# Optimization experiments

Measured on AMD Instinct MI355X. Metric: run time of the kernel, lower is better.

## Reference

```python
import jax, jax.numpy as jnp
import numpy as np

# ---- shape constants (d_data=1, expand_factor=1) ----
B, L, DD = 32, 8192, 1
M, NL = 3, 2                      # 3 Mamba control nets, n_layers=2 each
DM = 4 * DD                       # mamba d_model = 4*d_data
DI = DM                           # d_inner = expand_factor * d_model
NS = 16                           # d_state
KC = 4                            # d_conv
DR = max(1, -(-DM // 16))         # dt_rank = ceil(d_model/16)
DT = 1e-4                         # forward scalar arg dt (fixed python float)
TAU = 1000.0
SMOOTH = int(round(0.001 / DT))   # smooth_len/dt = 10

# 9-point (8th order) central finite-difference coefficients for f' (no 1/dt)
_C1 = [1/280, -4/105, 1/5, -4/5, 0.0, 4/5, -1/5, 4/105, -1/280]

def deriv_approx_dy(x):
    Lp = x.shape[1] - 8
    return sum(c * x[:, k:k + Lp, :] for k, c in enumerate(_C1) if c != 0.0)

def smooth(x, k):
    # centered box filter, same output length (via cumsum sliding window)
    if k <= 1:
        return x
    xp = jnp.pad(x, ((0, 0), ((k - 1) // 2 + 1, k // 2), (0, 0)))
    c = jnp.cumsum(xp, axis=1)
    return (c[:, k:, :] - c[:, :-k, :]) / k

def rmsnorm(x, w):
    return x * jax.lax.rsqrt(jnp.mean(x * x, -1, keepdims=True) + 1e-5) * w

def causal_conv(u, w, b):
    # depthwise causal conv == torch Conv1d(groups=DI, padding=KC-1)[..., :L]
    Lc = u.shape[1]
    up = jnp.pad(u, ((0, 0), (KC - 1, 0), (0, 0)))
    y = sum(up[:, j:j + Lc, :] * w[:, j] for j in range(KC))
    return y + b

def selective_scan(u, delta, A, Bm, Cm, Dp):
    # u, delta: [b,l,di]; A: [di,ns]; Bm, Cm: [b,l,ns]; Dp: [di]
    dA = jnp.exp(delta[..., None] * A)                         # [b,l,di,ns]
    dBu = delta[..., None] * Bm[:, :, None, :] * u[..., None]  # [b,l,di,ns]
    def step(h, xs):
        a, bu = xs
        h = a * h + bu
        return h, h
    h0 = jnp.zeros((u.shape[0], DI, NS), u.dtype)
    _, hs = jax.lax.scan(step, h0, (jnp.moveaxis(dA, 1, 0), jnp.moveaxis(dBu, 1, 0)))
    hs = jnp.moveaxis(hs, 0, 1)                                # [b,l,di,ns]
    return jnp.einsum('bldn,bln->bld', hs, Cm) + u * Dp

def _run_mamba(x_in, m, in_proj_w, conv_w, conv_b, x_proj_w,
               dt_proj_w, dt_proj_b, A_log, D_param, norm_w, out_proj_w):
    h = x_in
    for l in range(NL):
        hn = rmsnorm(h, norm_w[m, l])
        xz = hn @ in_proj_w[m, l].T                            # [b,l,2*di]
        xc, res = jnp.split(xz, 2, axis=-1)
        xc = jax.nn.silu(causal_conv(xc, conv_w[m, l], conv_b[m, l]))
        dbc = xc @ x_proj_w[m, l].T
        dtr, Bm, Cm = dbc[..., :DR], dbc[..., DR:DR + NS], dbc[..., DR + NS:]
        delta = jax.nn.softplus(dtr @ dt_proj_w[m, l].T + dt_proj_b[m, l])
        A = -jnp.exp(A_log[m, l])
        y = selective_scan(xc, delta, A, Bm, Cm, D_param[m, l])
        y = y * jax.nn.silu(res)
        h = y @ out_proj_w[m, l].T + h                         # residual block
    return h

def _forward(x, in_proj_w, conv_w, conv_b, x_proj_w, dt_proj_w, dt_proj_b,
             A_log, D_param, norm_w, out_proj_w, omega_w, omega_b,
             gamma_w, gamma_b, d_w, d_b, b_param):
    xdot = deriv_approx_dy(x)                                  # [B, L-8, DD]
    z = jnp.concatenate([x[:, 4:-4, :], xdot], axis=-1)        # [B, L', 2]
    x_in = jnp.concatenate([z, jnp.flip(z, axis=1)], axis=-1)  # [B, L', 4]
    args = (in_proj_w, conv_w, conv_b, x_proj_w, dt_proj_w, dt_proj_b,
            A_log, D_param, norm_w, out_proj_w)
    omegaC = _run_mamba(x_in, 0, *args)
    gammaC = _run_mamba(x_in, 1, *args)
    dC = _run_mamba(x_in, 2, *args)
    b = jax.nn.relu(b_param) / TAU
    d = jax.nn.relu(dC @ d_w.T + d_b)
    omega = omegaC @ omega_w.T + omega_b
    gamma = (gammaC @ gamma_w.T + gamma_b) / TAU
    d = smooth(jnp.abs(d), SMOOTH)
    omega = smooth(jnp.abs(omega), SMOOTH)
    gamma = smooth(gamma, SMOOTH)
    z = jnp.concatenate([z[:, :, :-1], z[:, :, -1:] / DT], axis=-1)
    z1, z2 = z[:, :, :1], z[:, :, 1:]
    yhat = -omega ** 2 * z1 + gamma * z2 - b * (z1 ** 2) * z2 - d
    def pen(t):
        # torch.var(dim=1) is unbiased -> ddof=1
        return jnp.mean(jnp.var(jnp.diff(t, axis=1)[:, 1:, :], axis=1, ddof=1))
    penalty = (pen(omega) + pen(gamma) + pen(d)) / 3.0
    controls = jnp.concatenate([omegaC, gammaC, dC], axis=-1)
    return yhat, controls, penalty

def setup_inputs():
    key = jax.random.key(0)
    ks = jax.random.split(key, 16)
    f32 = jnp.float32
    def nrm(k, shape, s=0.1):
        return s * jax.random.normal(k, shape, f32)
    x = jax.random.normal(ks[0], (B, L, DD), f32)
    A_log = jnp.log(jnp.broadcast_to(jnp.arange(1, NS + 1, dtype=f32), (M, NL, DI, NS)))
    return {
        "x": x,
        "in_proj_w": nrm(ks[1], (M, NL, 2 * DI, DM)),
        "conv_w": nrm(ks[2], (M, NL, DI, KC)),
        "conv_b": nrm(ks[3], (M, NL, DI)),
        "x_proj_w": nrm(ks[4], (M, NL, DR + 2 * NS, DI)),
        "dt_proj_w": nrm(ks[5], (M, NL, DI, DR)),
        "dt_proj_b": nrm(ks[6], (M, NL, DI)),
        "A_log": A_log,
        "D_param": jnp.ones((M, NL, DI), f32),
        "norm_w": jnp.ones((M, NL, DM), f32),
        "out_proj_w": nrm(ks[7], (M, NL, DM, DI)),
        "omega_w": nrm(ks[8], (DD, DM)),
        "omega_b": nrm(ks[9], (DD,)),
        "gamma_w": nrm(ks[10], (DD, DM)),
        "gamma_b": nrm(ks[11], (DD,)),
        "d_w": nrm(ks[12], (DD, DM)),
        "d_b": nrm(ks[13], (DD,)),
        "b_param": jax.random.uniform(ks[14], (1,), f32),
    }

def reference(x, in_proj_w, conv_w, conv_b, x_proj_w, dt_proj_w, dt_proj_b,
              A_log, D_param, norm_w, out_proj_w, omega_w, omega_b,
              gamma_w, gamma_b, d_w, d_b, b_param):
    return _forward(x, in_proj_w, conv_w, conv_b, x_proj_w, dt_proj_w, dt_proj_b,
                    A_log, D_param, norm_w, out_proj_w, omega_w, omega_b,
                    gamma_w, gamma_b, d_w, d_b, b_param)
```

## Files before the change

### kernel.cpp

```cpp
#include <hip/hip_runtime.h>
#include <math.h>

#define Bn_   32
#define Ln_   8192
#define LCn   8184
#define NLn   2
#define NCHn  341
#define CHn   24
#define NGn   24

static constexpr long N_BL = (long)Bn_ * LCn;

static constexpr long OFF_H    = 0;
static constexpr long OFF_REC  = 12*N_BL;
static constexpr long OFF_YB   = 36*N_BL;
static constexpr long OFF_RAW  = OFF_REC;
static constexpr long OFF_PART = OFF_REC + 3*N_BL;

#define L2E_  1.4426950408889634f
#define LN2_  0.6931471805599453f
#define EXP2_(x) __builtin_amdgcn_exp2f(x)
#define LOG2_(x) __builtin_amdgcn_logf(x)

__device__ __forceinline__ float si_(float v) {
    float e = EXP2_(-v * L2E_);
    return v * __builtin_amdgcn_rcpf(1.f + e);
}

__device__ __forceinline__ float sel4(float4 v, int d) {
    return (d & 2) ? ((d & 1) ? v.w : v.z) : ((d & 1) ? v.y : v.x);
}

__device__ __forceinline__ float rowsum16(float p) {
    p += __int_as_float(__builtin_amdgcn_update_dpp(0, __float_as_int(p), 0x128, 0xF, 0xF, true));
    p += __int_as_float(__builtin_amdgcn_update_dpp(0, __float_as_int(p), 0x124, 0xF, 0xF, true));
    p += __int_as_float(__builtin_amdgcn_update_dpp(0, __float_as_int(p), 0x122, 0xF, 0xF, true));
    p += __int_as_float(__builtin_amdgcn_update_dpp(0, __float_as_int(p), 0x121, 0xF, 0xF, true));
    return p;
}

__global__ void k_prep(const float* __restrict__ x, float* __restrict__ xin) {
    long idx = (long)blockIdx.x * 256 + threadIdx.x;
    if (idx >= N_BL) return;
    int b = (int)(idx / LCn);
    int t = (int)(idx - (long)b * LCn);
    const float* xb = x + (long)b * Ln_;
    const float c0 = 1.f/280.f, c1 = -4.f/105.f, c2 = 0.2f, c3 = -0.8f,
                c5 = 0.8f, c6 = -0.2f, c7 = 4.f/105.f, c8 = -1.f/280.f;
    float xd  = c0*xb[t]   + c1*xb[t+1] + c2*xb[t+2] + c3*xb[t+3]
              + c5*xb[t+5] + c6*xb[t+6] + c7*xb[t+7] + c8*xb[t+8];
    float z0  = xb[t+4];
    int tf = LCn - 1 - t;
    float xdf = c0*xb[tf]   + c1*xb[tf+1] + c2*xb[tf+2] + c3*xb[tf+3]
              + c5*xb[tf+5] + c6*xb[tf+6] + c7*xb[tf+7] + c8*xb[tf+8];
    float zf0 = xb[tf+4];
    float4 v; v.x = z0; v.y = xd; v.z = zf0; v.w = xdf;
    *(float4*)(xin + idx*4) = v;
}

__global__ void k_preconv(const float* __restrict__ hin, long mstride, int l,
                          const float* __restrict__ ipw, const float* __restrict__ cw,
                          const float* __restrict__ cbv, const float* __restrict__ nw,
                          const float* __restrict__ xpw, const float* __restrict__ dtw,
                          const float* __restrict__ dtb, float* __restrict__ rec) {
    long idx = (long)blockIdx.x * 256 + threadIdx.x;
    if (idx >= 3*N_BL) return;
    int m = (int)(idx / N_BL);
    long r = idx - (long)m * N_BL;
    int bb = (int)(r / LCn);
    int t  = (int)(r - (long)bb * LCn);
    int ml = m*NLn + l;
    const float* hb = hin + (long)m*mstride + (long)bb*LCn*4;
    const float* W  = ipw + (long)ml*32;
    const float* wn = nw  + ml*4;
    const float* wc = cw  + ml*16;
    const float* bc = cbv + ml*4;
    float acc0=0.f, acc1=0.f, acc2=0.f, acc3=0.f;
#pragma unroll
    for (int j = 0; j < 4; j++) {
        int tt = t - 3 + j;
        if (tt < 0) continue;
        float4 hv = *(const float4*)(hb + (long)tt*4);
        float ms = (hv.x*hv.x + hv.y*hv.y + hv.z*hv.z + hv.w*hv.w)*0.25f + 1e-5f;
        float rs = __builtin_amdgcn_rsqf(ms);
        float hn0 = hv.x*rs*wn[0], hn1 = hv.y*rs*wn[1];
        float hn2 = hv.z*rs*wn[2], hn3 = hv.w*rs*wn[3];
        float x0 = W[0]*hn0 + W[1]*hn1 + W[2]*hn2 + W[3]*hn3;
        float x1 = W[4]*hn0 + W[5]*hn1 + W[6]*hn2 + W[7]*hn3;
        float x2 = W[8]*hn0 + W[9]*hn1 + W[10]*hn2 + W[11]*hn3;
        float x3 = W[12]*hn0 + W[13]*hn1 + W[14]*hn2 + W[15]*hn3;
        acc0 = fmaf(x0, wc[0*4+j], acc0);
        acc1 = fmaf(x1, wc[1*4+j], acc1);
        acc2 = fmaf(x2, wc[2*4+j], acc2);
        acc3 = fmaf(x3, wc[3*4+j], acc3);
    }
    float4 o;
    o.x = si_(acc0 + bc[0]); o.y = si_(acc1 + bc[1]);
    o.z = si_(acc2 + bc[2]); o.w = si_(acc3 + bc[3]);
    const float* P = xpw + (long)ml*33*4;
    float dtr = o.x*P[0] + o.y*P[1] + o.z*P[2] + o.w*P[3];
    const float* dwv = dtw + ml*4;
    const float* dbv = dtb + ml*4;
    float4 lg;
    lg.x = LOG2_(1.f + EXP2_(fmaf(dtr, dwv[0], dbv[0]) * L2E_));
    lg.y = LOG2_(1.f + EXP2_(fmaf(dtr, dwv[1], dbv[1]) * L2E_));
    lg.z = LOG2_(1.f + EXP2_(fmaf(dtr, dwv[2], dbv[2]) * L2E_));
    lg.w = LOG2_(1.f + EXP2_(fmaf(dtr, dwv[3], dbv[3]) * L2E_));
    float* rp = rec + ((long)m*N_BL + r)*8;
    *(float4*)rp       = o;
    *(float4*)(rp + 4) = lg;
}

__global__ __launch_bounds__(256, 8)
void k_scanB(const float* __restrict__ rec, int l,
             const float* __restrict__ xpw, const float* __restrict__ Alog,
             float* __restrict__ Ap, float* __restrict__ Sv) {
    int wid  = blockIdx.x*4 + (threadIdx.x >> 6);
    int lane = threadIdx.x & 63;
    int chunk = wid % NCHn;
    int g     = wid / NCHn;
    int m = g >> 3;
    int s = lane >> 4, n = lane & 15;
    int bb = (g & 7)*4 + s;
    int ml = m*NLn + l;
    const float* P  = xpw + (long)ml*33*4;
    const float* PB = P + (1+n)*4;
    float pb0 = PB[0]*LN2_, pb1 = PB[1]*LN2_, pb2 = PB[2]*LN2_, pb3 = PB[3]*LN2_;
    const float* AL = Alog + (long)ml*64 + n;
    float4 Av;
    Av.x = -EXP2_(AL[0]  * L2E_);
    Av.y = -EXP2_(AL[16] * L2E_);
    Av.z = -EXP2_(AL[32] * L2E_);
    Av.w = -EXP2_(AL[48] * L2E_);
    const float* rb = rec + ((long)m*N_BL + (long)bb*LCn)*8;
    int t0 = chunk*CHn;
    float4 ap; ap.x = ap.y = ap.z = ap.w = 1.f;
    float4 sv; sv.x = sv.y = sv.z = sv.w = 0.f;
#pragma unroll 4
    for (int t = t0; t < t0 + CHn; t++) {
        float4 u  = *(const float4*)(rb + (long)t*8);
        float4 lg = *(const float4*)(rb + (long)t*8 + 4);
        float Bv = u.x*pb0 + u.y*pb1 + u.z*pb2 + u.w*pb3;
        float4 a;
        a.x = EXP2_(lg.x * Av.x); a.y = EXP2_(lg.y * Av.y);
        a.z = EXP2_(lg.z * Av.z); a.w = EXP2_(lg.w * Av.w);
        sv.x = fmaf(a.x, sv.x, lg.x*u.x*Bv);
        sv.y = fmaf(a.y, sv.y, lg.y*u.y*Bv);
        sv.z = fmaf(a.z, sv.z, lg.z*u.z*Bv);
        sv.w = fmaf(a.w, sv.w, lg.w*u.w*Bv);
        ap.x *= a.x; ap.y *= a.y; ap.z *= a.z; ap.w *= a.w;
    }
    long ci = (((long)g*NCHn + chunk)*64 + lane)*4;
    *(float4*)(Ap + ci) = ap;
    *(float4*)(Sv + ci) = sv;
}

#define SCANC_G 8
__global__ __launch_bounds__(256)
void k_scanC(const float* __restrict__ Ap, float* __restrict__ Sv) {
    int g   = blockIdx.x;
    int tid = threadIdx.x;
    long base = (long)g*NCHn*256 + tid;
    const int NFULL = NCHn / SCANC_G;
    float h = 0.f;
    float ca[SCANC_G], cs[SCANC_G], na[SCANC_G], ns[SCANC_G];
#pragma unroll
    for (int j = 0; j < SCANC_G; j++) {
        ca[j] = Ap[base + (long)j*256];
        cs[j] = Sv[base + (long)j*256];
    }
    for (int grp = 0; grp < NFULL; grp++) {
        long gb = base + (long)grp*SCANC_G*256;
        if (grp + 1 < NFULL) {
            long nb = gb + (long)SCANC_G*256;
#pragma unroll
            for (int j = 0; j < SCANC_G; j++) {
                na[j] = Ap[nb + (long)j*256];
                ns[j] = Sv[nb + (long)j*256];
            }
        }
#pragma unroll
        for (int j = 0; j < SCANC_G; j++) {
            Sv[gb + (long)j*256] = h;
            h = fmaf(ca[j], h, cs[j]);
        }
#pragma unroll
        for (int j = 0; j < SCANC_G; j++) { ca[j] = na[j]; cs[j] = ns[j]; }
    }
    for (int cc = NFULL*SCANC_G; cc < NCHn; cc++) {
        long ci = base + (long)cc*256;
        float a = Ap[ci];
        float s = Sv[ci];
        Sv[ci] = h;
        h = fmaf(a, h, s);
    }
}

__global__ __launch_bounds__(256, 8)
void k_scanD(const float* __restrict__ rec, float* __restrict__ yb, int l,
             const float* __restrict__ xpw, const float* __restrict__ Alog,
             const float* __restrict__ H0, const float* __restrict__ Dp) {
    int wid  = blockIdx.x*4 + (threadIdx.x >> 6);
    int lane = threadIdx.x & 63;
    int chunk = wid % NCHn;
    int g     = wid / NCHn;
    int m = g >> 3;
    int s = lane >> 4, n = lane & 15;
    int bb = (g & 7)*4 + s;
    int ml = m*NLn + l;
    const float* P  = xpw + (long)ml*33*4;
    const float* PB = P + (1+n)*4;
    float pb0 = PB[0]*LN2_, pb1 = PB[1]*LN2_, pb2 = PB[2]*LN2_, pb3 = PB[3]*LN2_;
    const float* PC = P + (17+n)*4;
    float pc0 = PC[0], pc1 = PC[1], pc2 = PC[2], pc3 = PC[3];
    const float* AL = Alog + (long)ml*64 + n;
    float4 Av;
    Av.x = -EXP2_(AL[0]  * L2E_);
    Av.y = -EXP2_(AL[16] * L2E_);
    Av.z = -EXP2_(AL[32] * L2E_);
    Av.w = -EXP2_(AL[48] * L2E_);
    float Dd = Dp[ml*4 + (n & 3)];
    float4 h = *(const float4*)(H0 + (((long)g*NCHn + chunk)*64 + lane)*4);
    const float* rb = rec + ((long)m*N_BL + (long)bb*LCn)*8;
    float* ym = yb + ((long)m*N_BL + (long)bb*LCn)*4;
    int t0 = chunk*CHn;
#pragma unroll 4
    for (int t = t0; t < t0 + CHn; t++) {
        float4 u  = *(const float4*)(rb + (long)t*8);
        float4 lg = *(const float4*)(rb + (long)t*8 + 4);
        float Bv = u.x*pb0 + u.y*pb1 + u.z*pb2 + u.w*pb3;
        float Cv = u.x*pc0 + u.y*pc1 + u.z*pc2 + u.w*pc3;
        float4 a;
        a.x = EXP2_(lg.x * Av.x); a.y = EXP2_(lg.y * Av.y);
        a.z = EXP2_(lg.z * Av.z); a.w = EXP2_(lg.w * Av.w);
        h.x = fmaf(a.x, h.x, lg.x*u.x*Bv);
        h.y = fmaf(a.y, h.y, lg.y*u.y*Bv);
        h.z = fmaf(a.z, h.z, lg.z*u.z*Bv);
        h.w = fmaf(a.w, h.w, lg.w*u.w*Bv);
        float px = rowsum16(h.x * Cv);
        float py = rowsum16(h.y * Cv);
        float pz = rowsum16(h.z * Cv);
        float pw = rowsum16(h.w * Cv);
        if (n < 4) {
            float out = (n & 2) ? ((n & 1) ? pw : pz) : ((n & 1) ? py : px);
            float ud  = sel4(u, n);
            ym[(long)t*4 + n] = fmaf(ud, Dd, out);
        }
    }
}

__global__ void k_post(const float* __restrict__ hin, long mstride,
                       float* __restrict__ h, const float* __restrict__ yb, int l,
                       const float* __restrict__ ipw, const float* __restrict__ nw,
                       const float* __restrict__ opw) {
    long idx = (long)blockIdx.x * 256 + threadIdx.x;
    if (idx >= 3*N_BL) return;
    int m = (int)(idx / N_BL);
    long r = idx - (long)m * N_BL;
    int ml = m*NLn + l;
    float4 hv = *(const float4*)(hin + (long)m*mstride + r*4);
    float ms = (hv.x*hv.x + hv.y*hv.y + hv.z*hv.z + hv.w*hv.w)*0.25f + 1e-5f;
    float rs = __builtin_amdgcn_rsqf(ms);
    const float* wn = nw + ml*4;
    float hn0 = hv.x*rs*wn[0], hn1 = hv.y*rs*wn[1];
    float hn2 = hv.z*rs*wn[2], hn3 = hv.w*rs*wn[3];
    const float* W = ipw + (long)(ml*8 + 4)*4;
    float4 yv = *(const float4*)(yb + ((long)m*N_BL + r)*4);
    float g0 = yv.x * si_(W[0]*hn0  + W[1]*hn1  + W[2]*hn2  + W[3]*hn3);
    float g1 = yv.y * si_(W[4]*hn0  + W[5]*hn1  + W[6]*hn2  + W[7]*hn3);
    float g2 = yv.z * si_(W[8]*hn0  + W[9]*hn1  + W[10]*hn2 + W[11]*hn3);
    float g3 = yv.w * si_(W[12]*hn0 + W[13]*hn1 + W[14]*hn2 + W[15]*hn3);
    const float* O = opw + ml*16;
    float4 o;
    o.x = O[0]*g0  + O[1]*g1  + O[2]*g2  + O[3]*g3  + hv.x;
    o.y = O[4]*g0  + O[5]*g1  + O[6]*g2  + O[7]*g3  + hv.y;
    o.z = O[8]*g0  + O[9]*g1  + O[10]*g2 + O[11]*g3 + hv.z;
    o.w = O[12]*g0 + O[13]*g1 + O[14]*g2 + O[15]*g3 + hv.w;
    *(float4*)(h + (long)m*4*N_BL + r*4) = o;
}

__global__ void k_postHead(const float* __restrict__ hin,
                           const float* __restrict__ yb,
                           const float* __restrict__ ipw, const float* __restrict__ nw,
                           const float* __restrict__ opw,
                           const float* __restrict__ ww, const float* __restrict__ wb,
                           const float* __restrict__ gw, const float* __restrict__ gb,
                           const float* __restrict__ dw, const float* __restrict__ dbp,
                           float* __restrict__ raw, float* __restrict__ dout) {
    long r = (long)blockIdx.x * 256 + threadIdx.x;
    if (r >= N_BL) return;
    float4 om[3];
#pragma unroll
    for (int m = 0; m < 3; m++) {
        int ml = m*NLn + 1;
        float4 hv = *(const float4*)(hin + (long)m*4*N_BL + r*4);
        float ms = (hv.x*hv.x + hv.y*hv.y + hv.z*hv.z + hv.w*hv.w)*0.25f + 1e-5f;
        float rs = __builtin_amdgcn_rsqf(ms);
        const float* wn = nw + ml*4;
        float hn0 = hv.x*rs*wn[0], hn1 = hv.y*rs*wn[1];
        float hn2 = hv.z*rs*wn[2], hn3 = hv.w*rs*wn[3];
        const float* W = ipw + (long)(ml*8 + 4)*4;
        float4 yv = *(const float4*)(yb + ((long)m*N_BL + r)*4);
        float g0 = yv.x * si_(W[0]*hn0  + W[1]*hn1  + W[2]*hn2  + W[3]*hn3);
        float g1 = yv.y * si_(W[4]*hn0  + W[5]*hn1  + W[6]*hn2  + W[7]*hn3);
        float g2 = yv.z * si_(W[8]*hn0  + W[9]*hn1  + W[10]*hn2 + W[11]*hn3);
        float g3 = yv.w * si_(W[12]*hn0 + W[13]*hn1 + W[14]*hn2 + W[15]*hn3);
        const float* O = opw + ml*16;
        float4 o;
        o.x = O[0]*g0  + O[1]*g1  + O[2]*g2  + O[3]*g3  + hv.x;
        o.y = O[4]*g0  + O[5]*g1  + O[6]*g2  + O[7]*g3  + hv.y;
        o.z = O[8]*g0  + O[9]*g1  + O[10]*g2 + O[11]*g3 + hv.z;
        o.w = O[12]*g0 + O[13]*g1 + O[14]*g2 + O[15]*g3 + hv.w;
        om[m] = o;
    }
    float4* c = (float4*)(dout + N_BL + r*12);
    c[0] = om[0]; c[1] = om[1]; c[2] = om[2];
    raw[r]          = om[0].x*ww[0] + om[0].y*ww[1] + om[0].z*ww[2] + om[0].w*ww[3] + wb[0];
    raw[N_BL + r]   = (om[1].x*gw[0] + om[1].y*gw[1] + om[1].z*gw[2] + om[1].w*gw[3] + gb[0]) / 1000.0f;
    raw[2*N_BL + r] = fmaxf(om[2].x*dw[0] + om[2].y*dw[1] + om[2].z*dw[2] + om[2].w*dw[3] + dbp[0], 0.f);
}

__global__ __launch_bounds__(256)
void k_smoothpen(const float* __restrict__ x, const float* __restrict__ raw,
                 const float* __restrict__ bp, float* __restrict__ dout,
                 double* __restrict__ part) {
    int b    = blockIdx.x >> 5;
    int tile = blockIdx.x & 31;
    int k    = threadIdx.x;
    int t0   = tile << 8;
    int t    = t0 + k;
    __shared__ float so_[257], sg_[257], sd_[257];
    const float* ro = raw + (long)b*LCn;
    const float* rg = raw + N_BL   + (long)b*LCn;
    const float* rd = raw + 2*N_BL + (long)b*LCn;
    auto smo3 = [&](int tt, float& o, float& g, float& d) {
        o = g = d = 0.f;
        if (tt < 0 || tt >= LCn) return;
        int lo = max(tt - 4, 0), hi = min(tt + 5, LCn - 1);
        for (int q = lo; q <= hi; q++) {
            o += fabsf(ro[q]); g += rg[q]; d += fabsf(rd[q]);
        }
        o *= 0.1f; g *= 0.1f; d *= 0.1f;
    };
    float so, sg, sd;
    smo3(t, so, sg, sd);
    so_[k] = so; sg_[k] = sg; sd_[k] = sd;
    if (k == 0) {
        float a, bq, cq;
        smo3(t0 + 256, a, bq, cq);
        so_[256] = a; sg_[256] = bq; sd_[256] = cq;
    }
    __syncthreads();
    if (t < LCn) {
        const float* xb = x + (long)b * Ln_;
        const float c0 = 1.f/280.f, c1 = -4.f/105.f, c2 = 0.2f, c3 = -0.8f,
                    c5 = 0.8f, c6 = -0.2f, c7 = 4.f/105.f, c8 = -1.f/280.f;
        float xd  = c0*xb[t]   + c1*xb[t+1] + c2*xb[t+2] + c3*xb[t+3]
                  + c5*xb[t+5] + c6*xb[t+6] + c7*xb[t+7] + c8*xb[t+8];
        float z1 = xb[t+4];
        float z2 = xd / 0.0001f;
        float bq = fmaxf(bp[0], 0.f) / 1000.0f;
        dout[(long)b*LCn + t] = -so*so*z1 + sg*z2 - bq*z1*z1*z2 - sd;
    }
    double v[6] = {0,0,0,0,0,0};
    if (t >= 1 && t <= LCn - 2) {
        double go = (double)so_[k+1] - (double)so_[k];
        double gg = (double)sg_[k+1] - (double)sg_[k];
        double gd = (double)sd_[k+1] - (double)sd_[k];
        v[0] = go; v[1] = go*go;
        v[2] = gg; v[3] = gg*gg;
        v[4] = gd; v[5] = gd*gd;
    }
#pragma unroll
    for (int j = 0; j < 6; j++) {
        for (int off = 32; off > 0; off >>= 1)
            v[j] += __shfl_down(v[j], off, 64);
    }
    __shared__ double wsum[4][6];
    int w = threadIdx.x >> 6;
    if ((threadIdx.x & 63) == 0) {
#pragma unroll
        for (int j = 0; j < 6; j++) wsum[w][j] = v[j];
    }
    __syncthreads();
    if (threadIdx.x == 0) {
        double s[6];
#pragma unroll
        for (int j = 0; j < 6; j++)
            s[j] = wsum[0][j] + wsum[1][j] + wsum[2][j] + wsum[3][j];
        long pb = (((long)0*32 + b)*32 + tile)*2;
        part[pb]   = s[0]; part[pb+1] = s[1];
        pb = (((long)1*32 + b)*32 + tile)*2;
        part[pb]   = s[2]; part[pb+1] = s[3];
        pb = (((long)2*32 + b)*32 + tile)*2;
        part[pb]   = s[4]; part[pb+1] = s[5];
    }
}

__global__ void k_pen2(const double* __restrict__ part, float* __restrict__ pout) {
    int tid = threadIdx.x;
    double var = 0.0;
    if (tid < 96) {
        int which = tid / 32, b = tid % 32;
        double su = 0.0, s2 = 0.0;
        for (int tl = 0; tl < 32; tl++) {
            const double* p = part + (((long)which*32 + b)*32 + tl)*2;
            su += p[0]; s2 += p[1];
        }
        const double N = (double)(LCn - 2);
        var = (s2 - su*su/N) / (N - 1.0);
    }
    __shared__ double sh[128];
    sh[tid] = var;
    __syncthreads();
    for (int o = 64; o > 0; o >>= 1) {
        if (tid < o) sh[tid] += sh[tid + o];
        __syncthreads();
    }
    if (tid == 0) pout[0] = (float)(sh[0] / 96.0);
}

extern "C" void kernel_launch(void* const* d_in, const int* in_sizes, int n_in,
                              void* d_out, int out_size, void* d_ws, size_t ws_size,
                              hipStream_t stream) {
    const float* x    = (const float*)d_in[0];
    const float* ipw  = (const float*)d_in[1];
    const float* cw   = (const float*)d_in[2];
    const float* cbv  = (const float*)d_in[3];
    const float* xpw  = (const float*)d_in[4];
    const float* dtw  = (const float*)d_in[5];
    const float* dtb  = (const float*)d_in[6];
    const float* Alog = (const float*)d_in[7];
    const float* Dp   = (const float*)d_in[8];
    const float* nw   = (const float*)d_in[9];
    const float* opw  = (const float*)d_in[10];
    const float* ww   = (const float*)d_in[11];
    const float* wb   = (const float*)d_in[12];
    const float* gw   = (const float*)d_in[13];
    const float* gb   = (const float*)d_in[14];
    const float* dw   = (const float*)d_in[15];
    const float* dbp  = (const float*)d_in[16];
    const float* bp   = (const float*)d_in[17];

    float* ws   = (float*)d_ws;
    float* h    = ws + OFF_H;
    float* rec  = ws + OFF_REC;
    float* yb   = ws + OFF_YB;
    float* ap   = yb;
    float* raw  = ws + OFF_RAW;
    double* part = (double*)(ws + OFF_PART);
    float* dout = (float*)d_out;
    float* xin = dout;
    float* sv  = dout + 4*N_BL;

    hipLaunchKernelGGL(k_prep, dim3(1023), dim3(256), 0, stream, x, xin);
    for (int l = 0; l < NLn; l++) {
        const float* hin = (l == 0) ? xin : h;
        long mstride = (l == 0) ? 0L : 4*N_BL;
        hipLaunchKernelGGL(k_preconv, dim3(3069), dim3(256), 0, stream,
                           hin, mstride, l, ipw, cw, cbv, nw, xpw, dtw, dtb, rec);
        hipLaunchKernelGGL(k_scanB, dim3(2046), dim3(256), 0, stream,
                           rec, l, xpw, Alog, ap, sv);
        hipLaunchKernelGGL(k_scanC, dim3(NGn), dim3(256), 0, stream, ap, sv);
        hipLaunchKernelGGL(k_scanD, dim3(2046), dim3(256), 0, stream,
                           rec, yb, l, xpw, Alog, sv, Dp);
        if (l == 0) {
            hipLaunchKernelGGL(k_post, dim3(3069), dim3(256), 0, stream,
                               hin, mstride, h, yb, l, ipw, nw, opw);
        } else {
            hipLaunchKernelGGL(k_postHead, dim3(1023), dim3(256), 0, stream,
                               h, yb, ipw, nw, opw, ww, wb, gw, gb, dw, dbp, raw, dout);
        }
    }
    hipLaunchKernelGGL(k_smoothpen, dim3(1024), dim3(256), 0, stream,
                       x, raw, bp, dout, part);
    hipLaunchKernelGGL(k_pen2, dim3(1), dim3(128), 0, stream, part, dout + 13*N_BL);
}
```

Baseline: 199.2 us.

## Fuse prep, post and preconv stages into tiled kernels with shared-memory conv halo

```diff
diff --git a/kernel.cpp b/kernel.cpp
--- a/kernel.cpp
+++ b/kernel.cpp
@@ -39,64 +39,52 @@
     return p;
 }
 
-__global__ void k_prep(const float* __restrict__ x, float* __restrict__ xin) {
-    long idx = (long)blockIdx.x * 256 + threadIdx.x;
-    if (idx >= N_BL) return;
-    int b = (int)(idx / LCn);
-    int t = (int)(idx - (long)b * LCn);
-    const float* xb = x + (long)b * Ln_;
+__device__ __forceinline__ float4 compute_xin(const float* __restrict__ xb, int p) {
     const float c0 = 1.f/280.f, c1 = -4.f/105.f, c2 = 0.2f, c3 = -0.8f,
                 c5 = 0.8f, c6 = -0.2f, c7 = 4.f/105.f, c8 = -1.f/280.f;
-    float xd  = c0*xb[t]   + c1*xb[t+1] + c2*xb[t+2] + c3*xb[t+3]
-              + c5*xb[t+5] + c6*xb[t+6] + c7*xb[t+7] + c8*xb[t+8];
-    float z0  = xb[t+4];
-    int tf = LCn - 1 - t;
+    float xd  = c0*xb[p]   + c1*xb[p+1] + c2*xb[p+2] + c3*xb[p+3]
+              + c5*xb[p+5] + c6*xb[p+6] + c7*xb[p+7] + c8*xb[p+8];
+    int tf = LCn - 1 - p;
     float xdf = c0*xb[tf]   + c1*xb[tf+1] + c2*xb[tf+2] + c3*xb[tf+3]
               + c5*xb[tf+5] + c6*xb[tf+6] + c7*xb[tf+7] + c8*xb[tf+8];
-    float zf0 = xb[tf+4];
-    float4 v; v.x = z0; v.y = xd; v.z = zf0; v.w = xdf;
-    *(float4*)(xin + idx*4) = v;
-}
-
-__global__ void k_preconv(const float* __restrict__ hin, long mstride, int l,
-                          const float* __restrict__ ipw, const float* __restrict__ cw,
-                          const float* __restrict__ cbv, const float* __restrict__ nw,
-                          const float* __restrict__ xpw, const float* __restrict__ dtw,
-                          const float* __restrict__ dtb, float* __restrict__ rec) {
-    long idx = (long)blockIdx.x * 256 + threadIdx.x;
-    if (idx >= 3*N_BL) return;
-    int m = (int)(idx / N_BL);
-    long r = idx - (long)m * N_BL;
-    int bb = (int)(r / LCn);
-    int t  = (int)(r - (long)bb * LCn);
-    int ml = m*NLn + l;
-    const float* hb = hin + (long)m*mstride + (long)bb*LCn*4;
-    const float* W  = ipw + (long)ml*32;
-    const float* wn = nw  + ml*4;
+    float4 v; v.x = xb[p+4]; v.y = xd; v.z = xb[tf+4]; v.w = xdf;
+    return v;
+}
+
+__device__ __forceinline__ float4 rms_xproj(float4 hv, const float* __restrict__ wn,
+                                            const float* __restrict__ W) {
+    float ms = (hv.x*hv.x + hv.y*hv.y + hv.z*hv.z + hv.w*hv.w)*0.25f + 1e-5f;
+    float rs = __builtin_amdgcn_rsqf(ms);
+    float hn0 = hv.x*rs*wn[0], hn1 = hv.y*rs*wn[1];
+    float hn2 = hv.z*rs*wn[2], hn3 = hv.w*rs*wn[3];
+    float4 o;
+    o.x = W[0]*hn0  + W[1]*hn1  + W[2]*hn2  + W[3]*hn3;
+    o.y = W[4]*hn0  + W[5]*hn1  + W[6]*hn2  + W[7]*hn3;
+    o.z = W[8]*hn0  + W[9]*hn1  + W[10]*hn2 + W[11]*hn3;
+    o.w = W[12]*hn0 + W[13]*hn1 + W[14]*hn2 + W[15]*hn3;
+    return o;
+}
+
+__device__ __forceinline__ void conv_lg_store(const float4* xp, int k, int ml,
+                                              const float* __restrict__ cw,
+                                              const float* __restrict__ cbv,
+                                              const float* __restrict__ xpw,
+                                              const float* __restrict__ dtw,
+                                              const float* __restrict__ dtb,
+                                              float* __restrict__ rp) {
     const float* wc = cw  + ml*16;
     const float* bc = cbv + ml*4;
-    float acc0=0.f, acc1=0.f, acc2=0.f, acc3=0.f;
+    float acc0 = bc[0], acc1 = bc[1], acc2 = bc[2], acc3 = bc[3];
 #pragma unroll
     for (int j = 0; j < 4; j++) {
-        int tt = t - 3 + j;
-        if (tt < 0) continue;
-        float4 hv = *(const float4*)(hb + (long)tt*4);
-        float ms = (hv.x*hv.x + hv.y*hv.y + hv.z*hv.z + hv.w*hv.w)*0.25f + 1e-5f;
-        float rs = __builtin_amdgcn_rsqf(ms);
-        float hn0 = hv.x*rs*wn[0], hn1 = hv.y*rs*wn[1];
-        float hn2 = hv.z*rs*wn[2], hn3 = hv.w*rs*wn[3];
-        float x0 = W[0]*hn0 + W[1]*hn1 + W[2]*hn2 + W[3]*hn3;
-        float x1 = W[4]*hn0 + W[5]*hn1 + W[6]*hn2 + W[7]*hn3;
-        float x2 = W[8]*hn0 + W[9]*hn1 + W[10]*hn2 + W[11]*hn3;
-        float x3 = W[12]*hn0 + W[13]*hn1 + W[14]*hn2 + W[15]*hn3;
-        acc0 = fmaf(x0, wc[0*4+j], acc0);
-        acc1 = fmaf(x1, wc[1*4+j], acc1);
-        acc2 = fmaf(x2, wc[2*4+j], acc2);
-        acc3 = fmaf(x3, wc[3*4+j], acc3);
+        float4 xv = xp[k + j];
+        acc0 = fmaf(xv.x, wc[0*4+j], acc0);
+        acc1 = fmaf(xv.y, wc[1*4+j], acc1);
+        acc2 = fmaf(xv.z, wc[2*4+j], acc2);
+        acc3 = fmaf(xv.w, wc[3*4+j], acc3);
     }
     float4 o;
-    o.x = si_(acc0 + bc[0]); o.y = si_(acc1 + bc[1]);
-    o.z = si_(acc2 + bc[2]); o.w = si_(acc3 + bc[3]);
+    o.x = si_(acc0); o.y = si_(acc1); o.z = si_(acc2); o.w = si_(acc3);
     const float* P = xpw + (long)ml*33*4;
     float dtr = o.x*P[0] + o.y*P[1] + o.z*P[2] + o.w*P[3];
     const float* dwv = dtw + ml*4;
@@ -106,9 +94,92 @@
     lg.y = LOG2_(1.f + EXP2_(fmaf(dtr, dwv[1], dbv[1]) * L2E_));
     lg.z = LOG2_(1.f + EXP2_(fmaf(dtr, dwv[2], dbv[2]) * L2E_));
     lg.w = LOG2_(1.f + EXP2_(fmaf(dtr, dwv[3], dbv[3]) * L2E_));
-    float* rp = rec + ((long)m*N_BL + r)*8;
     *(float4*)rp       = o;
     *(float4*)(rp + 4) = lg;
+}
+
+__global__ __launch_bounds__(256)
+void k_pre0(const float* __restrict__ x,
+            const float* __restrict__ ipw, const float* __restrict__ cw,
+            const float* __restrict__ cbv, const float* __restrict__ nw,
+            const float* __restrict__ xpw, const float* __restrict__ dtw,
+            const float* __restrict__ dtb, float* __restrict__ rec) {
+    __shared__ float4 xp[259];
+    int blk = blockIdx.x;
+    int m = blk >> 10, bb = (blk >> 5) & 31, tile = blk & 31;
+    int ml = m*NLn;
+    int t0 = tile << 8, k = threadIdx.x;
+    int t  = t0 + k;
+    const float* xb = x + (long)bb*Ln_;
+    const float* W  = ipw + (long)ml*32;
+    const float* wn = nw  + ml*4;
+    auto G = [&](int p) -> float4 {
+        float4 o; o.x = o.y = o.z = o.w = 0.f;
+        if (p >= 0 && p < LCn) o = rms_xproj(compute_xin(xb, p), wn, W);
+        return o;
+    };
+    xp[k + 3] = G(t);
+    if (k < 3) xp[k] = G(t0 + k - 3);
+    __syncthreads();
+    if (t >= LCn) return;
+    conv_lg_store(xp, k, ml, cw, cbv, xpw, dtw, dtb,
+                  rec + ((long)m*N_BL + (long)bb*LCn + t)*8);
+}
+
+__global__ __launch_bounds__(256)
+void k_mid(const float* __restrict__ x, const float* __restrict__ yb,
+           float* __restrict__ hout,
+           const float* __restrict__ ipw, const float* __restrict__ cw,
+           const float* __restrict__ cbv, const float* __restrict__ nw,
+           const float* __restrict__ xpw, const float* __restrict__ dtw,
+           const float* __restrict__ dtb, const float* __restrict__ opw,
+           float* __restrict__ rec) {
+    __shared__ float4 xp[259];
+    int blk = blockIdx.x;
+    int m = blk >> 10, bb = (blk >> 5) & 31, tile = blk & 31;
+    int ml0 = m*NLn, ml1 = ml0 + 1;
+    int t0 = tile << 8, k = threadIdx.x;
+    int t  = t0 + k;
+    const float* xb  = x + (long)bb*Ln_;
+    const float* wn0 = nw + ml0*4;
+    const float* Wr  = ipw + (long)(ml0*8 + 4)*4;
+    const float* O   = opw + ml0*16;
+    const float* wn1 = nw + ml1*4;
+    const float* W1  = ipw + (long)ml1*32;
+    auto H = [&](int p) -> float4 {
+        float4 hv = compute_xin(xb, p);
+        float ms = (hv.x*hv.x + hv.y*hv.y + hv.z*hv.z + hv.w*hv.w)*0.25f + 1e-5f;
+        float rs = __builtin_amdgcn_rsqf(ms);
+        float hn0 = hv.x*rs*wn0[0], hn1 = hv.y*rs*wn0[1];
+        float hn2 = hv.z*rs*wn0[2], hn3 = hv.w*rs*wn0[3];
+        float4 yv = *(const float4*)(yb + ((long)m*N_BL + (long)bb*LCn + p)*4);
+        float g0 = yv.x * si_(Wr[0]*hn0  + Wr[1]*hn1  + Wr[2]*hn2  + Wr[3]*hn3);
+        float g1 = yv.y * si_(Wr[4]*hn0  + Wr[5]*hn1  + Wr[6]*hn2  + Wr[7]*hn3);
+        float g2 = yv.z * si_(Wr[8]*hn0  + Wr[9]*hn1  + Wr[10]*hn2 + Wr[11]*hn3);
+        float g3 = yv.w * si_(Wr[12]*hn0 + Wr[13]*hn1 + Wr[14]*hn2 + Wr[15]*hn3);
+        float4 o;
+        o.x = O[0]*g0  + O[1]*g1  + O[2]*g2  + O[3]*g3  + hv.x;
+        o.y = O[4]*g0  + O[5]*g1  + O[6]*g2  + O[7]*g3  + hv.y;
+        o.z = O[8]*g0  + O[9]*g1  + O[10]*g2 + O[11]*g3 + hv.z;
+        o.w = O[12]*g0 + O[13]*g1 + O[14]*g2 + O[15]*g3 + hv.w;
+        return o;
+    };
+    float4 zf; zf.x = zf.y = zf.z = zf.w = 0.f;
+    if (t < LCn) {
+        float4 hnew = H(t);
+        *(float4*)(hout + ((long)m*N_BL + (long)bb*LCn + t)*4) = hnew;
+        xp[k + 3] = rms_xproj(hnew, wn1, W1);
+    } else {
+        xp[k + 3] = zf;
+    }
+    if (k < 3) {
+        int p = t0 + k - 3;
+        xp[k] = (p >= 0) ? rms_xproj(H(p), wn1, W1) : zf;
+    }
+    __syncthreads();
+    if (t >= LCn) return;
+    conv_lg_store(xp, k, ml1, cw, cbv, xpw, dtw, dtb,
+                  rec + ((long)m*N_BL + (long)bb*LCn + t)*8);
 }
 
 __global__ __launch_bounds__(256, 8)
@@ -249,36 +320,6 @@
     }
 }
 
-__global__ void k_post(const float* __restrict__ hin, long mstride,
-                       float* __restrict__ h, const float* __restrict__ yb, int l,
-                       const float* __restrict__ ipw, const float* __restrict__ nw,
-                       const float* __restrict__ opw) {
-    long idx = (long)blockIdx.x * 256 + threadIdx.x;
-    if (idx >= 3*N_BL) return;
-    int m = (int)(idx / N_BL);
-    long r = idx - (long)m * N_BL;
-    int ml = m*NLn + l;
-    float4 hv = *(const float4*)(hin + (long)m*mstride + r*4);
-    float ms = (hv.x*hv.x + hv.y*hv.y + hv.z*hv.z + hv.w*hv.w)*0.25f + 1e-5f;
-    float rs = __builtin_amdgcn_rsqf(ms);
-    const float* wn = nw + ml*4;
-    float hn0 = hv.x*rs*wn[0], hn1 = hv.y*rs*wn[1];
-    float hn2 = hv.z*rs*wn[2], hn3 = hv.w*rs*wn[3];
-    const float* W = ipw + (long)(ml*8 + 4)*4;
-    float4 yv = *(const float4*)(yb + ((long)m*N_BL + r)*4);
-    float g0 = yv.x * si_(W[0]*hn0  + W[1]*hn1  + W[2]*hn2  + W[3]*hn3);
-    float g1 = yv.y * si_(W[4]*hn0  + W[5]*hn1  + W[6]*hn2  + W[7]*hn3);
-    float g2 = yv.z * si_(W[8]*hn0  + W[9]*hn1  + W[10]*hn2 + W[11]*hn3);
-    float g3 = yv.w * si_(W[12]*hn0 + W[13]*hn1 + W[14]*hn2 + W[15]*hn3);
-    const float* O = opw + ml*16;
-    float4 o;
-    o.x = O[0]*g0  + O[1]*g1  + O[2]*g2  + O[3]*g3  + hv.x;
-    o.y = O[4]*g0  + O[5]*g1  + O[6]*g2  + O[7]*g3  + hv.y;
-    o.z = O[8]*g0  + O[9]*g1  + O[10]*g2 + O[11]*g3 + hv.z;
-    o.w = O[12]*g0 + O[13]*g1 + O[14]*g2 + O[15]*g3 + hv.w;
-    *(float4*)(h + (long)m*4*N_BL + r*4) = o;
-}
-
 __global__ void k_postHead(const float* __restrict__ hin,
                            const float* __restrict__ yb,
                            const float* __restrict__ ipw, const float* __restrict__ nw,
@@ -450,28 +491,24 @@
     float* raw  = ws + OFF_RAW;
     double* part = (double*)(ws + OFF_PART);
     float* dout = (float*)d_out;
-    float* xin = dout;
     float* sv  = dout + 4*N_BL;
 
-    hipLaunchKernelGGL(k_prep, dim3(1023), dim3(256), 0, stream, x, xin);
-    for (int l = 0; l < NLn; l++) {
-        const float* hin = (l == 0) ? xin : h;
-        long mstride = (l == 0) ? 0L : 4*N_BL;
-        hipLaunchKernelGGL(k_preconv, dim3(3069), dim3(256), 0, stream,
-                           hin, mstride, l, ipw, cw, cbv, nw, xpw, dtw, dtb, rec);
-        hipLaunchKernelGGL(k_scanB, dim3(2046), dim3(256), 0, stream,
-                           rec, l, xpw, Alog, ap, sv);
-        hipLaunchKernelGGL(k_scanC, dim3(NGn), dim3(256), 0, stream, ap, sv);
-        hipLaunchKernelGGL(k_scanD, dim3(2046), dim3(256), 0, stream,
-                           rec, yb, l, xpw, Alog, sv, Dp);
-        if (l == 0) {
-            hipLaunchKernelGGL(k_post, dim3(3069), dim3(256), 0, stream,
-                               hin, mstride, h, yb, l, ipw, nw, opw);
-        } else {
-            hipLaunchKernelGGL(k_postHead, dim3(1023), dim3(256), 0, stream,
-                               h, yb, ipw, nw, opw, ww, wb, gw, gb, dw, dbp, raw, dout);
-        }
-    }
+    hipLaunchKernelGGL(k_pre0, dim3(3072), dim3(256), 0, stream,
+                       x, ipw, cw, cbv, nw, xpw, dtw, dtb, rec);
+    hipLaunchKernelGGL(k_scanB, dim3(2046), dim3(256), 0, stream,
+                       rec, 0, xpw, Alog, ap, sv);
+    hipLaunchKernelGGL(k_scanC, dim3(NGn), dim3(256), 0, stream, ap, sv);
+    hipLaunchKernelGGL(k_scanD, dim3(2046), dim3(256), 0, stream,
+                       rec, yb, 0, xpw, Alog, sv, Dp);
+    hipLaunchKernelGGL(k_mid, dim3(3072), dim3(256), 0, stream,
+                       x, yb, h, ipw, cw, cbv, nw, xpw, dtw, dtb, opw, rec);
+    hipLaunchKernelGGL(k_scanB, dim3(2046), dim3(256), 0, stream,
+                       rec, 1, xpw, Alog, ap, sv);
+    hipLaunchKernelGGL(k_scanC, dim3(NGn), dim3(256), 0, stream, ap, sv);
+    hipLaunchKernelGGL(k_scanD, dim3(2046), dim3(256), 0, stream,
+                       rec, yb, 1, xpw, Alog, sv, Dp);
+    hipLaunchKernelGGL(k_postHead, dim3(1023), dim3(256), 0, stream,
+                       h, yb, ipw, nw, opw, ww, wb, gw, gb, dw, dbp, raw, dout);
     hipLaunchKernelGGL(k_smoothpen, dim3(1024), dim3(256), 0, stream,
                        x, raw, bp, dout, part);
     hipLaunchKernelGGL(k_pen2, dim3(1), dim3(128), 0, stream, part, dout + 13*N_BL);
```

Result: faster. 177.8 us, median of 3 (-10.8%).
